# Kernel tuning notes

Hardware: AMD Instinct MI355X
Metric: run time of the kernel (lower is better)

The kernel has to match this reference:

```python
import jax, jax.numpy as jnp
import numpy as np

EMBED = 1024
HEADS = 16
HDIM = EMBED // HEADS
WIN = 14
RANK = 16
ALPHA = 32
MLP = 4 * EMBED


def setup_inputs() -> dict:
    key = jax.random.key(0)
    ks = jax.random.split(key, 10)
    s = 0.02
    return {
        "x": jax.random.normal(ks[0], (2, 64, 64, EMBED), jnp.float32),
        "norm1_g": jnp.ones((EMBED,), jnp.float32),
        "norm1_b": jnp.zeros((EMBED,), jnp.float32),
        "qkv_w": jax.random.normal(ks[1], (EMBED, 3 * EMBED), jnp.float32) * s,
        "qkv_b": jnp.zeros((3 * EMBED,), jnp.float32),
        "lora_a": jax.random.normal(ks[2], (EMBED, RANK), jnp.float32) * s,
        "lora_b": jax.random.normal(ks[3], (RANK, 3 * EMBED), jnp.float32) * s,
        "rel_pos_h": jax.random.normal(ks[4], (2 * WIN - 1, HDIM), jnp.float32) * s,
        "rel_pos_w": jax.random.normal(ks[5], (2 * WIN - 1, HDIM), jnp.float32) * s,
        "proj_w": jax.random.normal(ks[6], (EMBED, EMBED), jnp.float32) * s,
        "proj_b": jnp.zeros((EMBED,), jnp.float32),
        "norm2_g": jnp.ones((EMBED,), jnp.float32),
        "norm2_b": jnp.zeros((EMBED,), jnp.float32),
        "mlp_w1": jax.random.normal(ks[7], (EMBED, MLP), jnp.float32) * s,
        "mlp_b1": jnp.zeros((MLP,), jnp.float32),
        "mlp_w2": jax.random.normal(ks[8], (MLP, EMBED), jnp.float32) * s,
        "mlp_b2": jnp.zeros((EMBED,), jnp.float32),
    }


def layer_norm(x, g, b, eps=1e-6):
    mu = jnp.mean(x, axis=-1, keepdims=True)
    var = jnp.var(x, axis=-1, keepdims=True)
    return (x - mu) * jax.lax.rsqrt(var + eps) * g + b


def window_partition(x, w):
    B, H, W, C = x.shape
    ph, pw = (w - H % w) % w, (w - W % w) % w
    x = jnp.pad(x, ((0, 0), (0, ph), (0, pw), (0, 0)))
    Hp, Wp = H + ph, W + pw
    x = x.reshape(B, Hp // w, w, Wp // w, w, C)
    x = x.transpose(0, 1, 3, 2, 4, 5).reshape(-1, w, w, C)
    return x, (Hp, Wp)


def window_unpartition(x, w, pad_hw, hw):
    Hp, Wp = pad_hw
    H, W = hw
    B = x.shape[0] // (Hp // w * (Wp // w))
    x = x.reshape(B, Hp // w, Wp // w, w, w, -1)
    x = x.transpose(0, 1, 3, 2, 4, 5).reshape(B, Hp, Wp, -1)
    return x[:, :H, :W, :]


def _rel_table(rel_pos, size):
    # square windows, no interpolation: table is (2*size-1, dim)
    idx = jnp.arange(size)[:, None] - jnp.arange(size)[None, :] + (size - 1)
    return rel_pos[idx]  # (size, size, dim)


def reference(x, norm1_g, norm1_b, qkv_w, qkv_b, lora_a, lora_b,
              rel_pos_h, rel_pos_w, proj_w, proj_b, norm2_g, norm2_b,
              mlp_w1, mlp_b1, mlp_w2, mlp_b2):
    shortcut = x
    xn = layer_norm(x, norm1_g, norm1_b)
    h, w = xn.shape[1], xn.shape[2]
    xw, pad_hw = window_partition(xn, WIN)
    Bw, H, W, C = xw.shape
    N = H * W
    xf = xw.reshape(Bw, N, C)
    # QKV with LoRA injection: qkv(x) + (x @ A @ B) * alpha/rank
    qkv = xf @ qkv_w + qkv_b + (xf @ lora_a @ lora_b) * (ALPHA / RANK)
    qkv = qkv.reshape(Bw, N, 3, HEADS, HDIM).transpose(2, 0, 3, 1, 4)  # 3,Bw,h,N,d
    q, k, v = qkv[0], qkv[1], qkv[2]
    scale = HDIM ** -0.5
    attn = jnp.einsum('bhnd,bhmd->bhnm', q * scale, k)  # (Bw,heads,N,N)
    # decomposed relative position bias
    Rh = _rel_table(rel_pos_h, H)  # (H,H,d)
    Rw = _rel_table(rel_pos_w, W)  # (W,W,d)
    rq = q.reshape(Bw, HEADS, H, W, HDIM)
    rel_h = jnp.einsum('bhxyd,xkd->bhxyk', rq, Rh)  # (Bw,heads,H,W,H)
    rel_w = jnp.einsum('bhxyd,ykd->bhxyk', rq, Rw)  # (Bw,heads,H,W,W)
    attn = (attn.reshape(Bw, HEADS, H, W, H, W)
            + rel_h[..., :, None] + rel_w[..., None, :]).reshape(Bw, HEADS, N, N)
    attn = jax.nn.softmax(attn, axis=-1)
    out = jnp.einsum('bhnm,bhmd->bhnd', attn, v)
    out = out.reshape(Bw, HEADS, H, W, HDIM).transpose(0, 2, 3, 1, 4).reshape(Bw, H, W, C)
    out = out @ proj_w + proj_b
    out = window_unpartition(out, WIN, pad_hw, (h, w))
    x = shortcut + out
    # MLP with exact GELU (torch default)
    xn2 = layer_norm(x, norm2_g, norm2_b)
    hmid = jax.nn.gelu(xn2 @ mlp_w1 + mlp_b1, approximate=False)
    x = x + (hmid @ mlp_w2 + mlp_b2)
    return x
```

## Files before the change

### kernel.cpp

```cpp
#include <hip/hip_runtime.h>
#include <cstdint>
#include <cstddef>


typedef __bf16 bf16x8 __attribute__((ext_vector_type(8)));
typedef float f32x4 __attribute__((ext_vector_type(4)));

__device__ __forceinline__ unsigned short f2bf(float f) {
    unsigned u = __float_as_uint(f);
    u = (u + 0x7fffu + ((u >> 16) & 1u)) >> 16;
    return (unsigned short)u;
}
__device__ __forceinline__ float bf2f(unsigned short h) {
    return __uint_as_float(((unsigned)h) << 16);
}

#define GLDS16(gp, lp) __builtin_amdgcn_global_load_lds( \
    (__attribute__((address_space(1))) unsigned int*)(gp), \
    (__attribute__((address_space(3))) unsigned int*)(lp), 16, 0, 0)

__global__ __launch_bounds__(256) void weff_kernel(
    const float* __restrict__ W, const float* __restrict__ la,
    const float* __restrict__ lb, unsigned short* __restrict__ Wt)
{
    __shared__ float tile[32][33];
    __shared__ float lat[32][16];
    __shared__ float lbt[16][32];
    const int kb = blockIdx.x * 32, nb = blockIdx.y * 32;
    const int tn = threadIdx.x & 31, tk = threadIdx.x >> 5;
    for (int i = threadIdx.x; i < 32 * 16; i += 256)
        lat[i >> 4][i & 15] = la[(size_t)(kb + (i >> 4)) * 16 + (i & 15)];
    for (int i = threadIdx.x; i < 16 * 32; i += 256)
        lbt[i >> 5][i & 31] = lb[(size_t)(i >> 5) * 3072 + nb + (i & 31)];
#pragma unroll
    for (int i = 0; i < 4; ++i) {
        int k = tk + i * 8;
        tile[k][tn] = W[(size_t)(kb + k) * 3072 + nb + tn];
    }
    __syncthreads();
#pragma unroll
    for (int i = 0; i < 4; ++i) {
        int n = tk + i * 8;
        float acc = tile[tn][n];
#pragma unroll
        for (int r = 0; r < 16; ++r) acc += 2.0f * lat[tn][r] * lbt[r][n];
        Wt[(size_t)(nb + n) * 1024 + kb + tn] = f2bf(acc);
    }
}

__global__ __launch_bounds__(256) void transpose_bf16_kernel(
    const float* __restrict__ W, unsigned short* __restrict__ Wt,
    int Kdim, int Ndim)
{
    __shared__ float tile[32][33];
    const int kb = blockIdx.x * 32, nb = blockIdx.y * 32;
    const int tn = threadIdx.x & 31, tk = threadIdx.x >> 5;
#pragma unroll
    for (int i = 0; i < 4; ++i) {
        int k = tk + i * 8;
        tile[k][tn] = W[(size_t)(kb + k) * Ndim + nb + tn];
    }
    __syncthreads();
#pragma unroll
    for (int i = 0; i < 4; ++i) {
        int n = tk + i * 8;
        Wt[(size_t)(nb + n) * Kdim + kb + tn] = f2bf(tile[tn][n]);
    }
}

__global__ __launch_bounds__(256) void ln1_kernel(
    const float* __restrict__ x, const float* __restrict__ g,
    const float* __restrict__ b, unsigned short* __restrict__ out)
{
    const int blk = blockIdx.x;
    const int tid = threadIdx.x;
    const int bw = blk / 196, tok = blk - bw * 196;
    const int bat = bw / 25, rw = bw - bat * 25;
    const int wy = rw / 5, wx = rw - wy * 5;
    const int ty = tok / 14, tx = tok - ty * 14;
    const int y = wy * 14 + ty, xx = wx * 14 + tx;
    unsigned short* orow = out + (size_t)blk * 1024;
    if (y >= 64 || xx >= 64) {
        *(uint2*)(orow + tid * 4) = make_uint2(0u, 0u);
        return;
    }
    const float* irow = x + ((size_t)((bat * 64 + y) * 64 + xx)) * 1024;
    const float4 v = *(const float4*)(irow + tid * 4);
    float s = v.x + v.y + v.z + v.w;
    float ss = v.x * v.x + v.y * v.y + v.z * v.z + v.w * v.w;
    for (int o = 32; o > 0; o >>= 1) { s += __shfl_xor(s, o); ss += __shfl_xor(ss, o); }
    __shared__ float red[8];
    const int wave = tid >> 6, lane = tid & 63;
    if (lane == 0) { red[wave] = s; red[4 + wave] = ss; }
    __syncthreads();
    s = red[0] + red[1] + red[2] + red[3];
    ss = red[4] + red[5] + red[6] + red[7];
    const float mu = s * (1.0f / 1024.0f);
    const float var = ss * (1.0f / 1024.0f) - mu * mu;
    const float rstd = rsqrtf(var + 1e-6f);
    const float4 gv = *(const float4*)(g + tid * 4);
    const float4 bv = *(const float4*)(b + tid * 4);
    const float a0 = (v.x - mu) * rstd * gv.x + bv.x;
    const float a1 = (v.y - mu) * rstd * gv.y + bv.y;
    const float a2 = (v.z - mu) * rstd * gv.z + bv.z;
    const float a3 = (v.w - mu) * rstd * gv.w + bv.w;
    const unsigned r0 = (unsigned)f2bf(a0) | ((unsigned)f2bf(a1) << 16);
    const unsigned r1 = (unsigned)f2bf(a2) | ((unsigned)f2bf(a3) << 16);
    *(uint2*)(orow + tid * 4) = make_uint2(r0, r1);
}

__global__ __launch_bounds__(256) void ln2_kernel(
    const float* __restrict__ x, const float* __restrict__ g,
    const float* __restrict__ b, unsigned short* __restrict__ out)
{
    const int blk = blockIdx.x;
    const int tid = threadIdx.x;
    const float* irow = x + (size_t)blk * 1024;
    unsigned short* orow = out + (size_t)blk * 1024;
    const float4 v = *(const float4*)(irow + tid * 4);
    float s = v.x + v.y + v.z + v.w;
    float ss = v.x * v.x + v.y * v.y + v.z * v.z + v.w * v.w;
    for (int o = 32; o > 0; o >>= 1) { s += __shfl_xor(s, o); ss += __shfl_xor(ss, o); }
    __shared__ float red[8];
    const int wave = tid >> 6, lane = tid & 63;
    if (lane == 0) { red[wave] = s; red[4 + wave] = ss; }
    __syncthreads();
    s = red[0] + red[1] + red[2] + red[3];
    ss = red[4] + red[5] + red[6] + red[7];
    const float mu = s * (1.0f / 1024.0f);
    const float var = ss * (1.0f / 1024.0f) - mu * mu;
    const float rstd = rsqrtf(var + 1e-6f);
    const float4 gv = *(const float4*)(g + tid * 4);
    const float4 bv = *(const float4*)(b + tid * 4);
    const float a0 = (v.x - mu) * rstd * gv.x + bv.x;
    const float a1 = (v.y - mu) * rstd * gv.y + bv.y;
    const float a2 = (v.z - mu) * rstd * gv.z + bv.z;
    const float a3 = (v.w - mu) * rstd * gv.w + bv.w;
    const unsigned r0 = (unsigned)f2bf(a0) | ((unsigned)f2bf(a1) << 16);
    const unsigned r1 = (unsigned)f2bf(a2) | ((unsigned)f2bf(a3) << 16);
    *(uint2*)(orow + tid * 4) = make_uint2(r0, r1);
}

template <int EPI>
__global__ __launch_bounds__(256) void gemm_kernel(
    const unsigned short* __restrict__ A,
    const unsigned short* __restrict__ Bt,
    const float* __restrict__ bias,
    void* __restrict__ outp,
    const float* __restrict__ aux,
    int M, int K, int nbm, int nbn)
{
    __shared__ unsigned short As[2][128 * 32];
    __shared__ unsigned short Bs[2][128 * 32];
    const int tid = threadIdx.x;
    const int wave = tid >> 6, lane = tid & 63;
    const int lr = lane & 15, lq = lane >> 4;
    const int ss = (nbm + 7) >> 3;
    const int xcd = blockIdx.x & 7;
    const int s = blockIdx.x >> 3;
    const int nt = s / ss;
    const int m_loc = s - nt * ss;
    const int mt = xcd * ss + m_loc;
    if (mt >= nbm) return;
    const int m_base = mt * 128, n_base = nt * 128;
    const int wm = (wave >> 1) * 64, wn = (wave & 1) * 64;
    const int N = nbn * 128;

    const int c0 = tid, c1 = tid + 256;
    const int row0 = c0 >> 2, row1 = c1 >> 2;
    const int kc = (tid & 3) ^ ((tid >> 3) & 3);
    int ar0 = m_base + row0; ar0 = ar0 < M ? ar0 : M - 1;
    int ar1 = m_base + row1; ar1 = ar1 < M ? ar1 : M - 1;
    int br0 = n_base + row0; br0 = br0 < N ? br0 : N - 1;
    int br1 = n_base + row1; br1 = br1 < N ? br1 : N - 1;
    const unsigned short* agp0 = A + (size_t)ar0 * K + kc * 8;
    const unsigned short* agp1 = A + (size_t)ar1 * K + kc * 8;
    const unsigned short* bgp0 = Bt + (size_t)br0 * K + kc * 8;
    const unsigned short* bgp1 = Bt + (size_t)br1 * K + kc * 8;
    unsigned short* alp0 = As[0] + c0 * 8;
    unsigned short* alp1 = As[0] + c1 * 8;
    unsigned short* blp0 = Bs[0] + c0 * 8;
    unsigned short* blp1 = Bs[0] + c1 * 8;
    unsigned short* alp0b = As[1] + c0 * 8;
    unsigned short* alp1b = As[1] + c1 * 8;
    unsigned short* blp0b = Bs[1] + c0 * 8;
    unsigned short* blp1b = Bs[1] + c1 * 8;

    const int swz = (lq ^ ((lr >> 1) & 3)) * 8;

    f32x4 acc[4][4] = {};

    for (int k0 = 0; k0 < K; k0 += 64) {
        GLDS16(agp0 + k0, alp0);
        GLDS16(agp1 + k0, alp1);
        GLDS16(bgp0 + k0, blp0);
        GLDS16(bgp1 + k0, blp1);
        GLDS16(agp0 + k0 + 32, alp0b);
        GLDS16(agp1 + k0 + 32, alp1b);
        GLDS16(bgp0 + k0 + 32, blp0b);
        GLDS16(bgp1 + k0 + 32, blp1b);
        __syncthreads();
#pragma unroll
        for (int half = 0; half < 2; ++half) {
            bf16x8 af[4], bfr[4];
#pragma unroll
            for (int i = 0; i < 4; ++i) {
                af[i]  = *(const bf16x8*)(As[half] + (wm + i * 16 + lr) * 32 + swz);
                bfr[i] = *(const bf16x8*)(Bs[half] + (wn + i * 16 + lr) * 32 + swz);
            }
#pragma unroll
            for (int i = 0; i < 4; ++i)
#pragma unroll
                for (int j = 0; j < 4; ++j)
                    acc[i][j] = __builtin_amdgcn_mfma_f32_16x16x32_bf16(af[i], bfr[j], acc[i][j], 0, 0, 0);
        }
        __syncthreads();
    }

    float biasv[4];
#pragma unroll
    for (int j = 0; j < 4; ++j) biasv[j] = bias[n_base + wn + j * 16 + lr];

    if constexpr (EPI == 0) {
#pragma unroll
        for (int i = 0; i < 4; ++i) {
            const int m0i = m_base + wm + i * 16 + lq * 4;
            if (m0i >= M) continue;
            const int bw = m0i / 196, tok0 = m0i - bw * 196;
#pragma unroll
            for (int j = 0; j < 4; ++j) {
                const int n = n_base + wn + j * 16 + lr;
                const int which = n >> 10, hh = (n >> 6) & 15, d = n & 63;
                unsigned short* slotp = (unsigned short*)outp + (size_t)((bw * 3 + which) * 16 + hh) * 13312;
                if (which == 2) {
                    unsigned long long pv = 0;
#pragma unroll
                    for (int r = 0; r < 4; ++r)
                        pv |= (unsigned long long)f2bf(acc[i][j][r] + biasv[j]) << (16 * r);
                    *(unsigned long long*)(slotp + (size_t)d * 208 + tok0) = pv;
                } else {
#pragma unroll
                    for (int r = 0; r < 4; ++r)
                        slotp[(size_t)(tok0 + r) * 64 + d] = f2bf(acc[i][j][r] + biasv[j]);
                }
            }
        }
    } else {
#pragma unroll
        for (int i = 0; i < 4; ++i) {
#pragma unroll
            for (int r = 0; r < 4; ++r) {
                const int m = m_base + wm + i * 16 + lq * 4 + r;
                if (m >= M) continue;
                int y = 0, xx = 0, b = 0;
                if constexpr (EPI == 1) {
                    const int bw = m / 196, tok = m - bw * 196;
                    b = bw / 25;
                    const int rw = bw - b * 25;
                    const int wy = rw / 5, wx = rw - wy * 5;
                    const int ty = tok / 14, tx = tok - ty * 14;
                    y = wy * 14 + ty; xx = wx * 14 + tx;
                }
#pragma unroll
                for (int j = 0; j < 4; ++j) {
                    const int n = n_base + wn + j * 16 + lr;
                    const float v = acc[i][j][r] + biasv[j];
                    if constexpr (EPI == 1) {
                        if (y < 64 && xx < 64) {
                            const size_t idx = ((size_t)((b * 64 + y) * 64 + xx)) * 1024 + n;
                            ((float*)outp)[idx] = aux[idx] + v;
                        }
                    } else if constexpr (EPI == 2) {
                        const float t2 = 1.5957691216f * (v + 0.044715f * v * v * v);
                        const float e = __expf(-t2);
                        const float gl = v * __builtin_amdgcn_rcpf(1.0f + e);
                        ((unsigned short*)outp)[(size_t)m * 4096 + n] = f2bf(gl);
                    } else {
                        const size_t idx = (size_t)m * 1024 + n;
                        ((float*)outp)[idx] += v;
                    }
                }
            }
        }
    }
}

__global__ __launch_bounds__(256, 2) void attn_kernel(
    const unsigned short* __restrict__ qkv,
    const float* __restrict__ relh, const float* __restrict__ relw,
    unsigned short* __restrict__ attn_out)
{
    __shared__ unsigned short Vt[64][232];
    __shared__ unsigned short Pst[4][16][232];
    __shared__ unsigned short Db[196][28];

    const int tid = threadIdx.x;
    const int wave = tid >> 6, lane = tid & 63;
    const int lr = lane & 15, lq = lane >> 4;
    const int bw = blockIdx.x >> 4, h = blockIdx.x & 15;
    const unsigned short* qp = qkv + (size_t)((bw * 3 + 0) * 16 + h) * 13312;
    const unsigned short* kp = qkv + (size_t)((bw * 3 + 1) * 16 + h) * 13312;
    const unsigned short* vp = qkv + (size_t)((bw * 3 + 2) * 16 + h) * 13312;

    *(uint2*)&Pst[wave][lane >> 2][208 + (lane & 3) * 4] = make_uint2(0u, 0u);

    {
        unsigned short* vtf = &Vt[0][0];
        for (int idx = tid; idx < 64 * 29; idx += 256) {
            const int d = idx / 29, c = idx - d * 29;
            GLDS16(vp + d * 208 + c * 8, vtf + idx * 8);
        }
    }

    for (int t = wave; t < 28; t += 4) {
        const int isw = t >= 14;
        const int c = isw ? t - 14 : t;
        const int arow = isw ? (lr * 14 + c) : (c * 14 + lr);
        const unsigned short* ap = qp + arow * 64 + lq * 8;
        const bf16x8 a0 = *(const bf16x8*)ap;
        const bf16x8 a1 = *(const bf16x8*)(ap + 32);
        int ridx = c - lr + 13;
        ridx = ridx < 0 ? 0 : (ridx > 26 ? 26 : ridx);
        const float* tb = (isw ? relw : relh) + ridx * 64 + lq * 8;
        union BV { unsigned short u[8]; bf16x8 v; } b0, b1;
        {
            const float4 x0 = *(const float4*)tb;
            const float4 x1 = *(const float4*)(tb + 4);
            b0.u[0] = f2bf(x0.x); b0.u[1] = f2bf(x0.y); b0.u[2] = f2bf(x0.z); b0.u[3] = f2bf(x0.w);
            b0.u[4] = f2bf(x1.x); b0.u[5] = f2bf(x1.y); b0.u[6] = f2bf(x1.z); b0.u[7] = f2bf(x1.w);
            const float4 x2 = *(const float4*)(tb + 32);
            const float4 x3 = *(const float4*)(tb + 36);
            b1.u[0] = f2bf(x2.x); b1.u[1] = f2bf(x2.y); b1.u[2] = f2bf(x2.z); b1.u[3] = f2bf(x2.w);
            b1.u[4] = f2bf(x3.x); b1.u[5] = f2bf(x3.y); b1.u[6] = f2bf(x3.z); b1.u[7] = f2bf(x3.w);
        }
        f32x4 dacc = {};
        dacc = __builtin_amdgcn_mfma_f32_16x16x32_bf16(a0, b0.v, dacc, 0, 0, 0);
        dacc = __builtin_amdgcn_mfma_f32_16x16x32_bf16(a1, b1.v, dacc, 0, 0, 0);
#pragma unroll
        for (int r = 0; r < 4; ++r) {
            const int y = lq * 4 + r;
            if (y < 14 && lr < 14) {
                const int g = isw ? y * 14 + c : c * 14 + y;
                Db[g][isw ? 14 + lr : lr] = f2bf(dacc[r]);
            }
        }
    }
    __syncthreads();

    for (int mt = wave; mt < 13; mt += 4) {
        const int m0 = mt * 16;
        const unsigned short* qb = qp + (size_t)(m0 + lr) * 64 + lq * 8;
        const bf16x8 qa0 = *(const bf16x8*)qb;
        const bf16x8 qa1 = *(const bf16x8*)(qb + 32);
        f32x4 sc[13];
#pragma unroll
        for (int nt = 0; nt < 13; ++nt) {
            const unsigned short* kb = kp + (size_t)(nt * 16 + lr) * 64 + lq * 8;
            const bf16x8 k0 = *(const bf16x8*)kb;
            const bf16x8 k1 = *(const bf16x8*)(kb + 32);
            f32x4 a = {};
            a = __builtin_amdgcn_mfma_f32_16x16x32_bf16(qa0, k0, a, 0, 0, 0);
            a = __builtin_amdgcn_mfma_f32_16x16x32_bf16(qa1, k1, a, 0, 0, 0);
            sc[nt] = a;
        }
        int grow[4];
#pragma unroll
        for (int r = 0; r < 4; ++r) {
            int g = m0 + lq * 4 + r;
            grow[r] = g > 195 ? 195 : g;
        }
#pragma unroll
        for (int nt = 0; nt < 13; ++nt) {
            const int n = nt * 16 + lr;
            if (n < 196) {
                const int nx = n / 14, ny = n - nx * 14;
#pragma unroll
                for (int r = 0; r < 4; ++r)
                    sc[nt][r] = sc[nt][r] * 0.125f + bf2f(Db[grow[r]][nx]) + bf2f(Db[grow[r]][14 + ny]);
            } else {
#pragma unroll
                for (int r = 0; r < 4; ++r) sc[nt][r] = -1e30f;
            }
        }
        float rs[4];
#pragma unroll
        for (int r = 0; r < 4; ++r) {
            float mx = sc[0][r];
#pragma unroll
            for (int nt = 1; nt < 13; ++nt) mx = fmaxf(mx, sc[nt][r]);
            mx = fmaxf(mx, __shfl_xor(mx, 1));
            mx = fmaxf(mx, __shfl_xor(mx, 2));
            mx = fmaxf(mx, __shfl_xor(mx, 4));
            mx = fmaxf(mx, __shfl_xor(mx, 8));
            float s = 0.f;
#pragma unroll
            for (int nt = 0; nt < 13; ++nt) {
                const float e = __expf(sc[nt][r] - mx);
                sc[nt][r] = e;
                s += e;
            }
            s += __shfl_xor(s, 1);
            s += __shfl_xor(s, 2);
            s += __shfl_xor(s, 4);
            s += __shfl_xor(s, 8);
            rs[r] = 1.0f / s;
        }
#pragma unroll
        for (int nt = 0; nt < 13; ++nt)
#pragma unroll
            for (int r = 0; r < 4; ++r)
                Pst[wave][lq * 4 + r][nt * 16 + lr] = f2bf(sc[nt][r]);
#pragma unroll
        for (int dt = 0; dt < 4; ++dt) {
            f32x4 a = {};
#pragma unroll
            for (int ks = 0; ks < 7; ++ks) {
                const bf16x8 pa = *(const bf16x8*)&Pst[wave][lr][ks * 32 + lq * 8];
                const bf16x8 vb = *(const bf16x8*)&Vt[dt * 16 + lr][ks * 32 + lq * 8];
                a = __builtin_amdgcn_mfma_f32_16x16x32_bf16(pa, vb, a, 0, 0, 0);
            }
#pragma unroll
            for (int r = 0; r < 4; ++r) {
                const int m = m0 + lq * 4 + r;
                if (m < 196)
                    attn_out[(size_t)(bw * 196 + m) * 1024 + h * 64 + dt * 16 + lr] = f2bf(a[r] * rs[r]);
            }
        }
    }
}

extern "C" void kernel_launch(void* const* d_in, const int* in_sizes, int n_in,
                              void* d_out, int out_size, void* d_ws, size_t ws_size,
                              hipStream_t stream)
{
    (void)in_sizes; (void)n_in; (void)out_size; (void)ws_size;
    const float* x      = (const float*)d_in[0];
    const float* n1g    = (const float*)d_in[1];
    const float* n1b    = (const float*)d_in[2];
    const float* qkv_w  = (const float*)d_in[3];
    const float* qkv_b  = (const float*)d_in[4];
    const float* lora_a = (const float*)d_in[5];
    const float* lora_b = (const float*)d_in[6];
    const float* relh   = (const float*)d_in[7];
    const float* relw   = (const float*)d_in[8];
    const float* proj_w = (const float*)d_in[9];
    const float* proj_b = (const float*)d_in[10];
    const float* n2g    = (const float*)d_in[11];
    const float* n2b    = (const float*)d_in[12];
    const float* w1     = (const float*)d_in[13];
    const float* b1     = (const float*)d_in[14];
    const float* w2     = (const float*)d_in[15];
    const float* b2     = (const float*)d_in[16];
    float* out = (float*)d_out;

    char* ws = (char*)d_ws;
    size_t off = 0;
    auto alloc = [&](size_t bytes) {
        char* p = ws + off;
        off += (bytes + 255) & ~(size_t)255;
        return p;
    };
    unsigned short* weffT = (unsigned short*)alloc((size_t)3072 * 1024 * 2);
    unsigned short* projT = (unsigned short*)alloc((size_t)1024 * 1024 * 2);
    unsigned short* w1T   = (unsigned short*)alloc((size_t)4096 * 1024 * 2);
    unsigned short* w2T   = (unsigned short*)alloc((size_t)1024 * 4096 * 2);
    unsigned short* xnw   = (unsigned short*)alloc((size_t)9800 * 1024 * 2);
    unsigned short* qkvb  = (unsigned short*)alloc((size_t)8192 * 4096 * 2);
    unsigned short* attno = (unsigned short*)alloc((size_t)9800 * 1024 * 2);

    weff_kernel<<<dim3(32, 96), 256, 0, stream>>>(qkv_w, lora_a, lora_b, weffT);
    transpose_bf16_kernel<<<dim3(32, 32), 256, 0, stream>>>(proj_w, projT, 1024, 1024);
    transpose_bf16_kernel<<<dim3(32, 128), 256, 0, stream>>>(w1, w1T, 1024, 4096);
    transpose_bf16_kernel<<<dim3(128, 32), 256, 0, stream>>>(w2, w2T, 4096, 1024);
    ln1_kernel<<<9800, 256, 0, stream>>>(x, n1g, n1b, xnw);
    gemm_kernel<0><<<8 * 10 * 24, 256, 0, stream>>>(xnw, weffT, qkv_b, qkvb, nullptr, 9800, 1024, 77, 24);
    attn_kernel<<<800, 256, 0, stream>>>(qkvb, relh, relw, attno);
    gemm_kernel<1><<<8 * 10 * 8, 256, 0, stream>>>(attno, projT, proj_b, out, x, 9800, 1024, 77, 8);
    unsigned short* xn2 = xnw;
    ln2_kernel<<<8192, 256, 0, stream>>>(out, n2g, n2b, xn2);
    unsigned short* hmid = qkvb;
    gemm_kernel<2><<<8 * 8 * 32, 256, 0, stream>>>(xn2, w1T, b1, hmid, nullptr, 8192, 1024, 64, 32);
    gemm_kernel<3><<<8 * 8 * 8, 256, 0, stream>>>(hmid, w2T, b2, out, nullptr, 8192, 4096, 64, 8);
}
```

Baseline: 576.4 us.

## Replace GEMM with 8-wave 256-row tile kernel using interleaved prefetch pipeline

Swaps the 4-wave 128x128 GEMM for an 8-wave kernel with 256-row tiles and 256- or 128-wide N tiles. It stages the next K-tiles through global_load_lds, interleaved between MFMA phases, using explicit vmcnt waits, barriers and setprio hints. It also changes the LDS swizzle to cover 64-wide K rows. The aim is higher MFMA utilisation through larger tiles that reuse more operand data and through overlapping memory loads with compute. The cost is more LDS and register pressure, and bigger tiles waste more work on the ragged M=9800 edge.

```diff
diff --git a/kernel.cpp b/kernel.cpp
--- a/kernel.cpp
+++ b/kernel.cpp
@@ -141,8 +141,8 @@
     *(uint2*)(orow + tid * 4) = make_uint2(r0, r1);
 }
 
-template <int EPI>
-__global__ __launch_bounds__(256) void gemm_kernel(
+template <int BN, int EPI>
+__global__ __launch_bounds__(512, 2) void gemm8p(
     const unsigned short* __restrict__ A,
     const unsigned short* __restrict__ Bt,
     const float* __restrict__ bias,
@@ -150,72 +150,148 @@
     const float* __restrict__ aux,
     int M, int K, int nbm, int nbn)
 {
-    __shared__ unsigned short As[2][128 * 32];
-    __shared__ unsigned short Bs[2][128 * 32];
+    constexpr int AMF  = (BN == 256) ? 8 : 4;
+    constexpr int LB   = (BN == 256) ? 2 : 1;
+    constexpr int BHR  = BN / 2;
+    constexpr int ABUF = 256 * 64;
+    constexpr int BBUF = BN * 64;
+
+    __shared__ unsigned short As_s[2 * ABUF];
+    __shared__ unsigned short Bs_s[2 * BBUF];
+
     const int tid = threadIdx.x;
     const int wave = tid >> 6, lane = tid & 63;
     const int lr = lane & 15, lq = lane >> 4;
+
     const int ss = (nbm + 7) >> 3;
     const int xcd = blockIdx.x & 7;
-    const int s = blockIdx.x >> 3;
-    const int nt = s / ss;
-    const int m_loc = s - nt * ss;
+    const int sidx = blockIdx.x >> 3;
+    const int ntl = sidx / ss;
+    const int m_loc = sidx - ntl * ss;
     const int mt = xcd * ss + m_loc;
     if (mt >= nbm) return;
-    const int m_base = mt * 128, n_base = nt * 128;
-    const int wm = (wave >> 1) * 64, wn = (wave & 1) * 64;
-    const int N = nbn * 128;
-
-    const int c0 = tid, c1 = tid + 256;
-    const int row0 = c0 >> 2, row1 = c1 >> 2;
-    const int kc = (tid & 3) ^ ((tid >> 3) & 3);
-    int ar0 = m_base + row0; ar0 = ar0 < M ? ar0 : M - 1;
-    int ar1 = m_base + row1; ar1 = ar1 < M ? ar1 : M - 1;
-    int br0 = n_base + row0; br0 = br0 < N ? br0 : N - 1;
-    int br1 = n_base + row1; br1 = br1 < N ? br1 : N - 1;
-    const unsigned short* agp0 = A + (size_t)ar0 * K + kc * 8;
-    const unsigned short* agp1 = A + (size_t)ar1 * K + kc * 8;
-    const unsigned short* bgp0 = Bt + (size_t)br0 * K + kc * 8;
-    const unsigned short* bgp1 = Bt + (size_t)br1 * K + kc * 8;
-    unsigned short* alp0 = As[0] + c0 * 8;
-    unsigned short* alp1 = As[0] + c1 * 8;
-    unsigned short* blp0 = Bs[0] + c0 * 8;
-    unsigned short* blp1 = Bs[0] + c1 * 8;
-    unsigned short* alp0b = As[1] + c0 * 8;
-    unsigned short* alp1b = As[1] + c1 * 8;
-    unsigned short* blp0b = Bs[1] + c0 * 8;
-    unsigned short* blp1b = Bs[1] + c1 * 8;
-
-    const int swz = (lq ^ ((lr >> 1) & 3)) * 8;
-
-    f32x4 acc[4][4] = {};
-
-    for (int k0 = 0; k0 < K; k0 += 64) {
-        GLDS16(agp0 + k0, alp0);
-        GLDS16(agp1 + k0, alp1);
-        GLDS16(bgp0 + k0, blp0);
-        GLDS16(bgp1 + k0, blp1);
-        GLDS16(agp0 + k0 + 32, alp0b);
-        GLDS16(agp1 + k0 + 32, alp1b);
-        GLDS16(bgp0 + k0 + 32, blp0b);
-        GLDS16(bgp1 + k0 + 32, blp1b);
-        __syncthreads();
-#pragma unroll
-        for (int half = 0; half < 2; ++half) {
-            bf16x8 af[4], bfr[4];
-#pragma unroll
-            for (int i = 0; i < 4; ++i) {
-                af[i]  = *(const bf16x8*)(As[half] + (wm + i * 16 + lr) * 32 + swz);
-                bfr[i] = *(const bf16x8*)(Bs[half] + (wn + i * 16 + lr) * 32 + swz);
-            }
-#pragma unroll
-            for (int i = 0; i < 4; ++i)
-#pragma unroll
-                for (int j = 0; j < 4; ++j)
-                    acc[i][j] = __builtin_amdgcn_mfma_f32_16x16x32_bf16(af[i], bfr[j], acc[i][j], 0, 0, 0);
-        }
-        __syncthreads();
-    }
+    const int m_base = mt * 256, n_base = ntl * BN;
+
+    const int wm = (BN == 256) ? (wave >> 2) * 128 : (wave >> 1) * 64;
+    const int wn = (BN == 256) ? (wave & 3) * 64 : (wave & 1) * 64;
+
+    const unsigned short* a_src[2][2];
+#pragma unroll
+    for (int h = 0; h < 2; ++h)
+#pragma unroll
+        for (int i = 0; i < 2; ++i) {
+            const int p = i * 512 + tid;
+            const int row = h * 128 + (p >> 3), sl = p & 7;
+            const int g = (((sl >> 2) ^ (row & 1)) << 2) | ((sl & 3) ^ ((row >> 1) & 3));
+            int gr = m_base + row; gr = gr < M ? gr : M - 1;
+            a_src[h][i] = A + (size_t)gr * K + g * 8;
+        }
+    const unsigned short* b_src[2][2];
+#pragma unroll
+    for (int h = 0; h < 2; ++h)
+#pragma unroll
+        for (int i = 0; i < LB; ++i) {
+            const int p = i * 512 + tid;
+            const int row = h * BHR + (p >> 3), sl = p & 7;
+            const int g = (((sl >> 2) ^ (row & 1)) << 2) | ((sl & 3) ^ ((row >> 1) & 3));
+            b_src[h][i] = Bt + (size_t)(n_base + row) * K + g * 8;
+        }
+    unsigned short* const a_dst0 = As_s + tid * 8;
+    unsigned short* const b_dst0 = Bs_s + tid * 8;
+
+#define STAGE_A(kt, h) do { \
+        unsigned short* _d = a_dst0 + (((kt) & 1) ? ABUF : 0) + (h) * 8192; \
+        GLDS16(a_src[h][0] + (size_t)(kt) * 64, _d); \
+        GLDS16(a_src[h][1] + (size_t)(kt) * 64, _d + 4096); \
+    } while (0)
+#define STAGE_B(kt, h) do { \
+        unsigned short* _d = b_dst0 + (((kt) & 1) ? BBUF : 0) + (h) * (BHR * 64); \
+        GLDS16(b_src[h][0] + (size_t)(kt) * 64, _d); \
+        if constexpr (LB == 2) GLDS16(b_src[h][1] + (size_t)(kt) * 64, _d + 4096); \
+    } while (0)
+#define VMCNT_STEADY() do { \
+        if constexpr (BN == 256) asm volatile("s_waitcnt vmcnt(6)" ::: "memory"); \
+        else                     asm volatile("s_waitcnt vmcnt(5)" ::: "memory"); \
+    } while (0)
+
+    const int frsw = ((lr & 1) << 2) | (lq ^ ((lr >> 1) & 3));
+    const int a_off = (wm + lr) * 64 + frsw * 8;
+    const int b_off = (wn + lr) * 64 + frsw * 8;
+
+    f32x4 acc[AMF][4] = {};
+    const int NT = K >> 6;
+
+    STAGE_A(0, 0); STAGE_A(0, 1); STAGE_B(0, 0); STAGE_B(0, 1);
+    STAGE_A(1, 0); STAGE_A(1, 1); STAGE_B(1, 0);
+    VMCNT_STEADY();
+    __builtin_amdgcn_s_barrier();
+
+    for (int t = 0; t < NT; ++t) {
+        const unsigned short* Ab = As_s + (t & 1) * ABUF;
+        const unsigned short* Bb = Bs_s + (t & 1) * BBUF;
+        bf16x8 af[AMF][2], b0[2], b1[2], b2[2], b3[2];
+#pragma unroll
+        for (int mf = 0; mf < AMF; ++mf) {
+            af[mf][0] = *(const bf16x8*)(Ab + a_off + mf * 1024);
+            af[mf][1] = *(const bf16x8*)(Ab + (a_off ^ 32) + mf * 1024);
+        }
+        b0[0] = *(const bf16x8*)(Bb + b_off);
+        b0[1] = *(const bf16x8*)(Bb + (b_off ^ 32));
+        b1[0] = *(const bf16x8*)(Bb + b_off + 1024);
+        b1[1] = *(const bf16x8*)(Bb + (b_off ^ 32) + 1024);
+        if (t + 1 < NT) STAGE_B(t + 1, 1);
+        __builtin_amdgcn_s_barrier();
+        asm volatile("s_waitcnt lgkmcnt(0)" ::: "memory");
+        __builtin_amdgcn_s_setprio(1);
+#pragma unroll
+        for (int mf = 0; mf < AMF; ++mf) {
+            acc[mf][0] = __builtin_amdgcn_mfma_f32_16x16x32_bf16(af[mf][0], b0[0], acc[mf][0], 0, 0, 0);
+            acc[mf][0] = __builtin_amdgcn_mfma_f32_16x16x32_bf16(af[mf][1], b0[1], acc[mf][0], 0, 0, 0);
+        }
+        __builtin_amdgcn_s_setprio(0);
+        __builtin_amdgcn_s_barrier();
+        b2[0] = *(const bf16x8*)(Bb + b_off + 2048);
+        b2[1] = *(const bf16x8*)(Bb + (b_off ^ 32) + 2048);
+        if (t + 2 < NT) STAGE_A(t + 2, 0);
+        __builtin_amdgcn_s_barrier();
+        asm volatile("s_waitcnt lgkmcnt(0)" ::: "memory");
+        __builtin_amdgcn_s_setprio(1);
+#pragma unroll
+        for (int mf = 0; mf < AMF; ++mf) {
+            acc[mf][1] = __builtin_amdgcn_mfma_f32_16x16x32_bf16(af[mf][0], b1[0], acc[mf][1], 0, 0, 0);
+            acc[mf][1] = __builtin_amdgcn_mfma_f32_16x16x32_bf16(af[mf][1], b1[1], acc[mf][1], 0, 0, 0);
+        }
+        __builtin_amdgcn_s_setprio(0);
+        __builtin_amdgcn_s_barrier();
+        b3[0] = *(const bf16x8*)(Bb + b_off + 3072);
+        b3[1] = *(const bf16x8*)(Bb + (b_off ^ 32) + 3072);
+        if (t + 2 < NT) STAGE_A(t + 2, 1);
+        __builtin_amdgcn_s_barrier();
+        asm volatile("s_waitcnt lgkmcnt(0)" ::: "memory");
+        __builtin_amdgcn_s_setprio(1);
+#pragma unroll
+        for (int mf = 0; mf < AMF; ++mf) {
+            acc[mf][2] = __builtin_amdgcn_mfma_f32_16x16x32_bf16(af[mf][0], b2[0], acc[mf][2], 0, 0, 0);
+            acc[mf][2] = __builtin_amdgcn_mfma_f32_16x16x32_bf16(af[mf][1], b2[1], acc[mf][2], 0, 0, 0);
+        }
+        __builtin_amdgcn_s_setprio(0);
+        __builtin_amdgcn_s_barrier();
+        if (t + 2 < NT) STAGE_B(t + 2, 0);
+        __builtin_amdgcn_s_barrier();
+        __builtin_amdgcn_s_setprio(1);
+#pragma unroll
+        for (int mf = 0; mf < AMF; ++mf) {
+            acc[mf][3] = __builtin_amdgcn_mfma_f32_16x16x32_bf16(af[mf][0], b3[0], acc[mf][3], 0, 0, 0);
+            acc[mf][3] = __builtin_amdgcn_mfma_f32_16x16x32_bf16(af[mf][1], b3[1], acc[mf][3], 0, 0, 0);
+        }
+        __builtin_amdgcn_s_setprio(0);
+        if (t < NT - 2) { VMCNT_STEADY(); }
+        else if (t == NT - 2) { asm volatile("s_waitcnt vmcnt(0)" ::: "memory"); }
+        __builtin_amdgcn_s_barrier();
+    }
+#undef STAGE_A
+#undef STAGE_B
+#undef VMCNT_STEADY
 
     float biasv[4];
 #pragma unroll
@@ -223,7 +299,7 @@
 
     if constexpr (EPI == 0) {
 #pragma unroll
-        for (int i = 0; i < 4; ++i) {
+        for (int i = 0; i < AMF; ++i) {
             const int m0i = m_base + wm + i * 16 + lq * 4;
             if (m0i >= M) continue;
             const int bw = m0i / 196, tok0 = m0i - bw * 196;
@@ -247,7 +323,7 @@
         }
     } else {
 #pragma unroll
-        for (int i = 0; i < 4; ++i) {
+        for (int i = 0; i < AMF; ++i) {
 #pragma unroll
             for (int r = 0; r < 4; ++r) {
                 const int m = m_base + wm + i * 16 + lq * 4 + r;
@@ -473,12 +549,12 @@
     transpose_bf16_kernel<<<dim3(32, 128), 256, 0, stream>>>(w1, w1T, 1024, 4096);
     transpose_bf16_kernel<<<dim3(128, 32), 256, 0, stream>>>(w2, w2T, 4096, 1024);
     ln1_kernel<<<9800, 256, 0, stream>>>(x, n1g, n1b, xnw);
-    gemm_kernel<0><<<8 * 10 * 24, 256, 0, stream>>>(xnw, weffT, qkv_b, qkvb, nullptr, 9800, 1024, 77, 24);
+    gemm8p<256, 0><<<dim3(8 * 5 * 12), 512, 0, stream>>>(xnw, weffT, qkv_b, qkvb, nullptr, 9800, 1024, 39, 12);
     attn_kernel<<<800, 256, 0, stream>>>(qkvb, relh, relw, attno);
-    gemm_kernel<1><<<8 * 10 * 8, 256, 0, stream>>>(attno, projT, proj_b, out, x, 9800, 1024, 77, 8);
+    gemm8p<128, 1><<<dim3(8 * 5 * 8), 512, 0, stream>>>(attno, projT, proj_b, out, x, 9800, 1024, 39, 8);
     unsigned short* xn2 = xnw;
     ln2_kernel<<<8192, 256, 0, stream>>>(out, n2g, n2b, xn2);
     unsigned short* hmid = qkvb;
-    gemm_kernel<2><<<8 * 8 * 32, 256, 0, stream>>>(xn2, w1T, b1, hmid, nullptr, 8192, 1024, 64, 32);
-    gemm_kernel<3><<<8 * 8 * 8, 256, 0, stream>>>(hmid, w2T, b2, out, nullptr, 8192, 4096, 64, 8);
-}
+    gemm8p<256, 2><<<dim3(8 * 4 * 16), 512, 0, stream>>>(xn2, w1T, b1, hmid, nullptr, 8192, 1024, 32, 16);
+    gemm8p<128, 3><<<dim3(8 * 4 * 8), 512, 0, stream>>>(hmid, w2T, b2, out, nullptr, 8192, 4096, 32, 8);
+}
```

New measurement: 602.4 us. +4.5%, slower.

## Add 256x256-tile 8-wave bf16 GEMM with split-K for QKV and MLP GEMMs

Applied to the files above, without the earlier changes.

Adds a new GEMM kernel with 512 threads, 256x256 output tiles and 64-wide K steps double-buffered through direct global-to-LDS loads with swizzled addressing. The inner loop interleaves LDS fragment reads with MFMA groups, separated by barriers and setprio raises. The QKV and first MLP GEMMs switch to it, and the second MLP GEMM uses split-K of 2 with atomic float adds into the residual output. The aim is more data reuse per block and better overlap of loads with matrix math. The cost is a very large LDS footprint that limits occupancy, many barriers, and nondeterministic atomic accumulation.

```diff
diff --git a/kernel.cpp b/kernel.cpp
--- a/kernel.cpp
+++ b/kernel.cpp
@@ -141,6 +141,196 @@
     *(uint2*)(orow + tid * 4) = make_uint2(r0, r1);
 }
 
+template <int EPI, int KS>
+__global__ __launch_bounds__(512, 2) void gemm8p_v2(
+    const unsigned short* __restrict__ A,
+    const unsigned short* __restrict__ Bt,
+    const float* __restrict__ bias,
+    void* __restrict__ outp,
+    const float* __restrict__ aux,
+    int M, int K, int nbm, int nbn)
+{
+    constexpr int ABUF = 256 * 64;
+    constexpr int BBUF = 256 * 64;
+
+    __shared__ unsigned short As_s[2 * ABUF];
+    __shared__ unsigned short Bs_s[2 * BBUF];
+
+    const int tid = threadIdx.x;
+    const int wave = tid >> 6, lane = tid & 63;
+    const int lr = lane & 15, lq = lane >> 4;
+
+    const int ss = (nbm + 7) >> 3;
+    const int xcd = blockIdx.x & 7;
+    const int sidx = blockIdx.x >> 3;
+    const int ntl2 = sidx / ss;
+    const int m_loc = sidx - ntl2 * ss;
+    const int mt = xcd * ss + m_loc;
+    if (mt >= nbm) return;
+    int ks = 0, ntl = ntl2;
+    if constexpr (KS > 1) {
+        ks = ntl2 / nbn;
+        ntl = ntl2 - ks * nbn;
+    }
+    const int m_base = mt * 256, n_base = ntl * 256;
+    const int Kp = K / KS;
+    const int kb = ks * Kp;
+    const int NT = Kp >> 6;
+
+    const int wm = (wave >> 2) * 128;
+    const int wn = (wave & 3) * 64;
+
+    const unsigned short* a_src[4];
+    const unsigned short* b_src[4];
+#pragma unroll
+    for (int i = 0; i < 4; ++i) {
+        const int p = i * 512 + tid;
+        const int row = p >> 3, sl = p & 7;
+        const int g = (((sl >> 2) ^ (row & 1)) << 2) | ((sl & 3) ^ ((row >> 1) & 3));
+        int gr = m_base + row; gr = gr < M ? gr : M - 1;
+        a_src[i] = A + (size_t)gr * K + kb + g * 8;
+        b_src[i] = Bt + (size_t)(n_base + row) * K + kb + g * 8;
+    }
+
+#define STAGE_ALL(kt) do { \
+        unsigned short* _ad = As_s + (((kt) & 1) ? ABUF : 0) + tid * 8; \
+        unsigned short* _bd = Bs_s + (((kt) & 1) ? BBUF : 0) + tid * 8; \
+        GLDS16(a_src[0] + (size_t)(kt) * 64, _ad); \
+        GLDS16(b_src[0] + (size_t)(kt) * 64, _bd); \
+        GLDS16(a_src[1] + (size_t)(kt) * 64, _ad + 4096); \
+        GLDS16(b_src[1] + (size_t)(kt) * 64, _bd + 4096); \
+        GLDS16(a_src[2] + (size_t)(kt) * 64, _ad + 8192); \
+        GLDS16(b_src[2] + (size_t)(kt) * 64, _bd + 8192); \
+        GLDS16(a_src[3] + (size_t)(kt) * 64, _ad + 12288); \
+        GLDS16(b_src[3] + (size_t)(kt) * 64, _bd + 12288); \
+    } while (0)
+
+    const int frsw = ((lr & 1) << 2) | (lq ^ ((lr >> 1) & 3));
+    const int a_off = (wm + lr) * 64 + frsw * 8;
+    const int b_off = (wn + lr) * 64 + frsw * 8;
+
+    f32x4 acc[8][4] = {};
+
+    STAGE_ALL(0);
+    asm volatile("s_waitcnt vmcnt(0)" ::: "memory");
+    __builtin_amdgcn_s_barrier();
+
+    for (int t = 0; t < NT; ++t) {
+        const unsigned short* Ab = As_s + (t & 1) * ABUF;
+        const unsigned short* Bb = Bs_s + (t & 1) * BBUF;
+        bf16x8 afr[4], bfr[4];
+#pragma unroll
+        for (int mf = 0; mf < 4; ++mf) afr[mf] = *(const bf16x8*)(Ab + a_off + mf * 1024);
+#pragma unroll
+        for (int nf = 0; nf < 4; ++nf) bfr[nf] = *(const bf16x8*)(Bb + b_off + nf * 1024);
+        if (t + 1 < NT) STAGE_ALL(t + 1);
+        __builtin_amdgcn_s_barrier();
+        asm volatile("s_waitcnt lgkmcnt(0)" ::: "memory");
+        __builtin_amdgcn_s_setprio(1);
+#pragma unroll
+        for (int mf = 0; mf < 4; ++mf)
+#pragma unroll
+            for (int nf = 0; nf < 4; ++nf)
+                acc[mf][nf] = __builtin_amdgcn_mfma_f32_16x16x32_bf16(afr[mf], bfr[nf], acc[mf][nf], 0, 0, 0);
+        __builtin_amdgcn_s_setprio(0);
+        __builtin_amdgcn_s_barrier();
+#pragma unroll
+        for (int mf = 0; mf < 4; ++mf) afr[mf] = *(const bf16x8*)(Ab + a_off + (4 + mf) * 1024);
+        __builtin_amdgcn_s_barrier();
+        asm volatile("s_waitcnt lgkmcnt(0)" ::: "memory");
+        __builtin_amdgcn_s_setprio(1);
+#pragma unroll
+        for (int mf = 0; mf < 4; ++mf)
+#pragma unroll
+            for (int nf = 0; nf < 4; ++nf)
+                acc[4 + mf][nf] = __builtin_amdgcn_mfma_f32_16x16x32_bf16(afr[mf], bfr[nf], acc[4 + mf][nf], 0, 0, 0);
+        __builtin_amdgcn_s_setprio(0);
+        __builtin_amdgcn_s_barrier();
+#pragma unroll
+        for (int mf = 0; mf < 4; ++mf) afr[mf] = *(const bf16x8*)(Ab + (a_off ^ 32) + mf * 1024);
+#pragma unroll
+        for (int nf = 0; nf < 4; ++nf) bfr[nf] = *(const bf16x8*)(Bb + (b_off ^ 32) + nf * 1024);
+        __builtin_amdgcn_s_barrier();
+        asm volatile("s_waitcnt lgkmcnt(0)" ::: "memory");
+        __builtin_amdgcn_s_setprio(1);
+#pragma unroll
+        for (int mf = 0; mf < 4; ++mf)
+#pragma unroll
+            for (int nf = 0; nf < 4; ++nf)
+                acc[mf][nf] = __builtin_amdgcn_mfma_f32_16x16x32_bf16(afr[mf], bfr[nf], acc[mf][nf], 0, 0, 0);
+        __builtin_amdgcn_s_setprio(0);
+        __builtin_amdgcn_s_barrier();
+#pragma unroll
+        for (int mf = 0; mf < 4; ++mf) afr[mf] = *(const bf16x8*)(Ab + (a_off ^ 32) + (4 + mf) * 1024);
+        __builtin_amdgcn_s_barrier();
+        asm volatile("s_waitcnt lgkmcnt(0)" ::: "memory");
+        __builtin_amdgcn_s_setprio(1);
+#pragma unroll
+        for (int mf = 0; mf < 4; ++mf)
+#pragma unroll
+            for (int nf = 0; nf < 4; ++nf)
+                acc[4 + mf][nf] = __builtin_amdgcn_mfma_f32_16x16x32_bf16(afr[mf], bfr[nf], acc[4 + mf][nf], 0, 0, 0);
+        __builtin_amdgcn_s_setprio(0);
+        asm volatile("s_waitcnt vmcnt(0)" ::: "memory");
+        __builtin_amdgcn_s_barrier();
+    }
+#undef STAGE_ALL
+
+    float biasv[4];
+#pragma unroll
+    for (int j = 0; j < 4; ++j)
+        biasv[j] = (KS == 1 || ks == 0) ? bias[n_base + wn + j * 16 + lr] : 0.0f;
+
+    if constexpr (EPI == 0) {
+#pragma unroll
+        for (int i = 0; i < 8; ++i) {
+            const int m0i = m_base + wm + i * 16 + lq * 4;
+            if (m0i >= M) continue;
+            const int bw = m0i / 196, tok0 = m0i - bw * 196;
+#pragma unroll
+            for (int j = 0; j < 4; ++j) {
+                const int n = n_base + wn + j * 16 + lr;
+                const int which = n >> 10, hh = (n >> 6) & 15, d = n & 63;
+                unsigned short* slotp = (unsigned short*)outp + (size_t)((bw * 3 + which) * 16 + hh) * 13312;
+                if (which == 2) {
+                    unsigned long long pv = 0;
+#pragma unroll
+                    for (int r = 0; r < 4; ++r)
+                        pv |= (unsigned long long)f2bf(acc[i][j][r] + biasv[j]) << (16 * r);
+                    *(unsigned long long*)(slotp + (size_t)d * 208 + tok0) = pv;
+                } else {
+#pragma unroll
+                    for (int r = 0; r < 4; ++r)
+                        slotp[(size_t)(tok0 + r) * 64 + d] = f2bf(acc[i][j][r] + biasv[j]);
+                }
+            }
+        }
+    } else {
+#pragma unroll
+        for (int i = 0; i < 8; ++i) {
+#pragma unroll
+            for (int r = 0; r < 4; ++r) {
+                const int m = m_base + wm + i * 16 + lq * 4 + r;
+                if (m >= M) continue;
+#pragma unroll
+                for (int j = 0; j < 4; ++j) {
+                    const int n = n_base + wn + j * 16 + lr;
+                    const float v = acc[i][j][r] + biasv[j];
+                    if constexpr (EPI == 2) {
+                        const float t2 = 1.5957691216f * (v + 0.044715f * v * v * v);
+                        const float e = __expf(-t2);
+                        const float gl = v * __builtin_amdgcn_rcpf(1.0f + e);
+                        ((unsigned short*)outp)[(size_t)m * 4096 + n] = f2bf(gl);
+                    } else {
+                        atomicAdd(&((float*)outp)[(size_t)m * 1024 + n], v);
+                    }
+                }
+            }
+        }
+    }
+    (void)aux;
+}
+
 template <int EPI>
 __global__ __launch_bounds__(256) void gemm_kernel(
     const unsigned short* __restrict__ A,
@@ -221,64 +411,33 @@
 #pragma unroll
     for (int j = 0; j < 4; ++j) biasv[j] = bias[n_base + wn + j * 16 + lr];
 
-    if constexpr (EPI == 0) {
-#pragma unroll
-        for (int i = 0; i < 4; ++i) {
-            const int m0i = m_base + wm + i * 16 + lq * 4;
-            if (m0i >= M) continue;
-            const int bw = m0i / 196, tok0 = m0i - bw * 196;
+#pragma unroll
+    for (int i = 0; i < 4; ++i) {
+#pragma unroll
+        for (int r = 0; r < 4; ++r) {
+            const int m = m_base + wm + i * 16 + lq * 4 + r;
+            if (m >= M) continue;
+            int y = 0, xx = 0, b = 0;
+            if constexpr (EPI == 1) {
+                const int bw = m / 196, tok = m - bw * 196;
+                b = bw / 25;
+                const int rw = bw - b * 25;
+                const int wy = rw / 5, wx = rw - wy * 5;
+                const int ty = tok / 14, tx = tok - ty * 14;
+                y = wy * 14 + ty; xx = wx * 14 + tx;
+            }
 #pragma unroll
             for (int j = 0; j < 4; ++j) {
                 const int n = n_base + wn + j * 16 + lr;
-                const int which = n >> 10, hh = (n >> 6) & 15, d = n & 63;
-                unsigned short* slotp = (unsigned short*)outp + (size_t)((bw * 3 + which) * 16 + hh) * 13312;
-                if (which == 2) {
-                    unsigned long long pv = 0;
-#pragma unroll
-                    for (int r = 0; r < 4; ++r)
-                        pv |= (unsigned long long)f2bf(acc[i][j][r] + biasv[j]) << (16 * r);
-                    *(unsigned long long*)(slotp + (size_t)d * 208 + tok0) = pv;
+                const float v = acc[i][j][r] + biasv[j];
+                if constexpr (EPI == 1) {
+                    if (y < 64 && xx < 64) {
+                        const size_t idx = ((size_t)((b * 64 + y) * 64 + xx)) * 1024 + n;
+                        ((float*)outp)[idx] = aux[idx] + v;
+                    }
                 } else {
-#pragma unroll
-                    for (int r = 0; r < 4; ++r)
-                        slotp[(size_t)(tok0 + r) * 64 + d] = f2bf(acc[i][j][r] + biasv[j]);
-                }
-            }
-        }
-    } else {
-#pragma unroll
-        for (int i = 0; i < 4; ++i) {
-#pragma unroll
-            for (int r = 0; r < 4; ++r) {
-                const int m = m_base + wm + i * 16 + lq * 4 + r;
-                if (m >= M) continue;
-                int y = 0, xx = 0, b = 0;
-                if constexpr (EPI == 1) {
-                    const int bw = m / 196, tok = m - bw * 196;
-                    b = bw / 25;
-                    const int rw = bw - b * 25;
-                    const int wy = rw / 5, wx = rw - wy * 5;
-                    const int ty = tok / 14, tx = tok - ty * 14;
-                    y = wy * 14 + ty; xx = wx * 14 + tx;
-                }
-#pragma unroll
-                for (int j = 0; j < 4; ++j) {
-                    const int n = n_base + wn + j * 16 + lr;
-                    const float v = acc[i][j][r] + biasv[j];
-                    if constexpr (EPI == 1) {
-                        if (y < 64 && xx < 64) {
-                            const size_t idx = ((size_t)((b * 64 + y) * 64 + xx)) * 1024 + n;
-                            ((float*)outp)[idx] = aux[idx] + v;
-                        }
-                    } else if constexpr (EPI == 2) {
-                        const float t2 = 1.5957691216f * (v + 0.044715f * v * v * v);
-                        const float e = __expf(-t2);
-                        const float gl = v * __builtin_amdgcn_rcpf(1.0f + e);
-                        ((unsigned short*)outp)[(size_t)m * 4096 + n] = f2bf(gl);
-                    } else {
-                        const size_t idx = (size_t)m * 1024 + n;
-                        ((float*)outp)[idx] += v;
-                    }
+                    const size_t idx = (size_t)m * 1024 + n;
+                    ((float*)outp)[idx] += v;
                 }
             }
         }
@@ -473,12 +632,12 @@
     transpose_bf16_kernel<<<dim3(32, 128), 256, 0, stream>>>(w1, w1T, 1024, 4096);
     transpose_bf16_kernel<<<dim3(128, 32), 256, 0, stream>>>(w2, w2T, 4096, 1024);
     ln1_kernel<<<9800, 256, 0, stream>>>(x, n1g, n1b, xnw);
-    gemm_kernel<0><<<8 * 10 * 24, 256, 0, stream>>>(xnw, weffT, qkv_b, qkvb, nullptr, 9800, 1024, 77, 24);
+    gemm8p_v2<0, 1><<<dim3(8 * 5 * 12), 512, 0, stream>>>(xnw, weffT, qkv_b, qkvb, nullptr, 9800, 1024, 39, 12);
     attn_kernel<<<800, 256, 0, stream>>>(qkvb, relh, relw, attno);
-    gemm_kernel<1><<<8 * 10 * 8, 256, 0, stream>>>(attno, projT, proj_b, out, x, 9800, 1024, 77, 8);
+    gemm_kernel<1><<<dim3(8 * 10 * 8), 256, 0, stream>>>(attno, projT, proj_b, out, x, 9800, 1024, 77, 8);
     unsigned short* xn2 = xnw;
     ln2_kernel<<<8192, 256, 0, stream>>>(out, n2g, n2b, xn2);
     unsigned short* hmid = qkvb;
-    gemm_kernel<2><<<8 * 8 * 32, 256, 0, stream>>>(xn2, w1T, b1, hmid, nullptr, 8192, 1024, 64, 32);
-    gemm_kernel<3><<<8 * 8 * 8, 256, 0, stream>>>(hmid, w2T, b2, out, nullptr, 8192, 4096, 64, 8);
-}
+    gemm8p_v2<2, 1><<<dim3(8 * 4 * 16), 512, 0, stream>>>(xn2, w1T, b1, hmid, nullptr, 8192, 1024, 32, 16);
+    gemm8p_v2<3, 2><<<dim3(8 * 4 * 8), 512, 0, stream>>>(hmid, w2T, b2, out, nullptr, 8192, 4096, 32, 4);
+}
```

Measured after the change: 597.1 us. +3.6%, slower.
